# Kernel optimization log

Hardware: AMD Instinct MI355X
Metric: run time of the kernel (lower is better)

## Reference

```python
import jax, jax.numpy as jnp
import numpy as np

N = 4096
F_IN = 512
F_OUT = 64
H = 8
ALPHA = 0.2
NEG_BIG = -9e15


def setup_inputs() -> dict:
    key = jax.random.key(0)
    ks = jax.random.split(key, 7)
    h = jax.random.normal(ks[0], (N, F_IN), dtype=jnp.float32)
    mask = jax.random.randint(ks[1], (N, N), 0, 2, dtype=jnp.int32)
    # per-head linear W: weight [H, F_IN, F_OUT], bias [H, F_OUT] (xavier-ish scale)
    w_scale = 1.414 * np.sqrt(6.0 / (F_IN + F_OUT))
    W = jax.random.uniform(ks[2], (H, F_IN, F_OUT), dtype=jnp.float32, minval=-w_scale, maxval=w_scale)
    bW = jnp.zeros((H, F_OUT), dtype=jnp.float32)
    # attention linear A: [2*F_OUT, 1] split into a_l (acts on Wh_i) and a_r (acts on Wh_j)
    a_scale = 1.414 * np.sqrt(6.0 / (2 * F_OUT + 1))
    a_l = jax.random.uniform(ks[3], (H, F_OUT), dtype=jnp.float32, minval=-a_scale, maxval=a_scale)
    a_r = jax.random.uniform(ks[4], (H, F_OUT), dtype=jnp.float32, minval=-a_scale, maxval=a_scale)
    bA = jnp.zeros((H,), dtype=jnp.float32)
    return {"h": h, "mask": mask, "W": W, "bW": bW, "a_l": a_l, "a_r": a_r, "bA": bA}


def reference(h, mask, W, bW, a_l, a_r, bA):
    # Wh: [H, N, F_OUT]
    Wh = jnp.einsum('ni,hio->hno', h, W) + bW[:, None, :]
    # A([Wh_i ; Wh_j]) decomposed as outer sum: e[h,i,j] = a_l.Wh_i + a_r.Wh_j + bA
    el = jnp.einsum('hno,ho->hn', Wh, a_l)  # [H, N]
    er = jnp.einsum('hno,ho->hn', Wh, a_r)  # [H, N]
    e = el[:, :, None] + er[:, None, :] + bA[:, None, None]  # [H, N, N]
    e = jax.nn.leaky_relu(e, negative_slope=ALPHA)
    e = jnp.where(mask[None] > 0, e, NEG_BIG)
    a = jax.nn.softmax(e, axis=-1)  # softmax over neighbors j (dim=1 in torch)
    # dropout omitted (eval mode / deterministic reference)
    aWh = jnp.einsum('hij,hjo->hio', a, Wh)  # [H, N, F_OUT]
    out = jax.nn.elu(aWh)  # last=False
    # concat heads along feature dim -> [N, H*F_OUT]
    return jnp.transpose(out, (1, 0, 2)).reshape(N, H * F_OUT)
```

## Files before the change

kernel.cpp:

```cpp
#include <hip/hip_runtime.h>
#include <hip/hip_bf16.h>
#include <hip/hip_fp16.h>

#define NN 4096
#define FIN 512
#define FOUT 64
#define NH 8
#define ALPHA 0.2f
#define PSCALE 4096.0f

typedef unsigned int uint;
typedef unsigned short ushort;
typedef unsigned char uchar;
typedef unsigned long long ull;
typedef __attribute__((ext_vector_type(8))) short short8;
typedef __attribute__((ext_vector_type(8))) _Float16 half8;
typedef __attribute__((ext_vector_type(4))) float floatx4;
typedef __attribute__((ext_vector_type(4))) uint uintx4;
typedef __attribute__((ext_vector_type(2))) uint uintx2;

__device__ __forceinline__ float bf2f(ushort s) { return __uint_as_float(((uint)s) << 16); }
__device__ __forceinline__ ushort f2bf(float f) {
    uint u = __float_as_uint(f);
    u += 0x7fffu + ((u >> 16) & 1u);
    return (ushort)(u >> 16);
}
__device__ __forceinline__ ushort f2h(float f) {
    return __half_as_ushort(__float2half_rn(f));
}

__device__ __forceinline__ int detect_bf16(const ushort* __restrict__ hraw) {
    int lane = threadIdx.x & 63;
    float a = fabsf(bf2f(hraw[2 * lane]));
    ull bal = __ballot(a >= 1e-3f && a <= 100.0f);
    return __popcll(bal) >= 32;
}

#define PM_BLKS 8192
#define CV_BLKS 1024
#define TW_BLKS 32

__global__ __launch_bounds__(256) void prep_kernel(
    const int* __restrict__ mask, uchar* __restrict__ mb,
    const void* __restrict__ hraw, ushort* __restrict__ bh,
    const void* __restrict__ Wraw, ushort* __restrict__ WT)
{
    const int b = blockIdx.x, t = threadIdx.x;
    if (b < PM_BLKS) {
        size_t gid = (size_t)b * 256 + t;
        const int* p = mask + gid * 8;
        int4 aa = *(const int4*)p;
        int4 bb = *(const int4*)(p + 4);
        uint by = (uint)(aa.x > 0)        | ((uint)(aa.y > 0) << 1)
                | ((uint)(aa.z > 0) << 2) | ((uint)(aa.w > 0) << 3)
                | ((uint)(bb.x > 0) << 4) | ((uint)(bb.y > 0) << 5)
                | ((uint)(bb.z > 0) << 6) | ((uint)(bb.w > 0) << 7);
        mb[gid] = (uchar)by;
    } else if (b < PM_BLKS + CV_BLKS) {
        int isbf = detect_bf16((const ushort*)hraw);
        size_t e0 = ((size_t)(b - PM_BLKS) * 256 + t) * 8;
        if (isbf) {
            *(uint4*)(bh + e0) = *(const uint4*)((const ushort*)hraw + e0);
        } else {
            const float* s = (const float*)hraw + e0;
            float4 f0 = *(const float4*)s;
            float4 f1 = *(const float4*)(s + 4);
            uint4 o;
            o.x = (uint)f2bf(f0.x) | ((uint)f2bf(f0.y) << 16);
            o.y = (uint)f2bf(f0.z) | ((uint)f2bf(f0.w) << 16);
            o.z = (uint)f2bf(f1.x) | ((uint)f2bf(f1.y) << 16);
            o.w = (uint)f2bf(f1.z) | ((uint)f2bf(f1.w) << 16);
            *(uint4*)(bh + e0) = o;
        }
    } else {
        int isbf = detect_bf16((const ushort*)hraw);
        int b2 = b - PM_BLKS - CV_BLKS;
        int h = b2 >> 2, kq = b2 & 3;
        int o = t & 63, sub = t >> 6;
        int kbase = kq * 128 + sub * 32;
        uint pk[16];
#pragma unroll
        for (int kk = 0; kk < 32; kk += 2) {
            float v0, v1;
            size_t s0 = ((size_t)h * FIN + kbase + kk) * FOUT + o;
            size_t s1 = s0 + FOUT;
            if (isbf) { v0 = bf2f(((const ushort*)Wraw)[s0]); v1 = bf2f(((const ushort*)Wraw)[s1]); }
            else      { v0 = ((const float*)Wraw)[s0];        v1 = ((const float*)Wraw)[s1]; }
            pk[kk >> 1] = (uint)f2bf(v0) | ((uint)f2bf(v1) << 16);
        }
        ushort* dst = WT + ((size_t)h * FOUT + o) * FIN + kbase;
#pragma unroll
        for (int q = 0; q < 4; q++)
            *(uint4*)(dst + q * 8) = make_uint4(pk[q*4], pk[q*4+1], pk[q*4+2], pk[q*4+3]);
    }
}

__global__ __launch_bounds__(256) void khv_kernel(const float* __restrict__ er,
                                                  float* __restrict__ Kh,
                                                  ushort* __restrict__ vt,
                                                  ushort* __restrict__ zt) {
    __shared__ float red[256];
    int h = blockIdx.x >> 3, sl = blockIdx.x & 7, t = threadIdx.x;
    float m = -3.0e38f;
    for (int j = t; j < NN; j += 256) m = fmaxf(m, er[(size_t)h * NN + j]);
    red[t] = m;
    __syncthreads();
    for (int s = 128; s >= 1; s >>= 1) {
        if (t < s) red[t] = fmaxf(red[t], red[t + s]);
        __syncthreads();
    }
    float kh = red[0];
    if (t == 0 && sl == 0) Kh[h] = kh;
    int j = sl * 512 + t;
#pragma unroll
    for (int q = 0; q < 2; q++, j += 256) {
        float d = er[(size_t)h * NN + j] - kh;
        vt[(size_t)h * NN + j] = f2h(__expf(d));
        zt[(size_t)h * NN + j] = f2h(__expf(ALPHA * d));
    }
}

__global__ __launch_bounds__(256) void wh_kernel(
    const ushort* __restrict__ hmat, const ushort* __restrict__ WT,
    const void* __restrict__ bWr, const void* __restrict__ alr,
    const void* __restrict__ arr, const void* __restrict__ bAr,
    const ushort* __restrict__ hraw,
    ushort* __restrict__ WhT, float* __restrict__ el, float* __restrict__ er)
{
    __shared__ __align__(16) ushort sT[64][72];
    const int t = threadIdx.x, lane = t & 63, wid = t >> 6;
    const int head = blockIdx.y, rbase = blockIdx.x * 64;
    const int lm = lane & 15, lq = lane >> 4;

    floatx4 C[4];
#pragma unroll
    for (int cg = 0; cg < 4; cg++) C[cg] = (floatx4){0.f, 0.f, 0.f, 0.f};

    const ushort* Ap = hmat + (size_t)(rbase + wid * 16 + lm) * FIN + lq * 8;
    const ushort* Bp = WT + (size_t)head * FOUT * FIN + (size_t)lm * FIN + lq * 8;

#pragma unroll
    for (int kc = 0; kc < 16; kc++) {
        short8 a = *(const short8*)(Ap + kc * 32);
#pragma unroll
        for (int cg = 0; cg < 4; cg++) {
            short8 b = *(const short8*)(Bp + (size_t)cg * 16 * FIN + kc * 32);
            C[cg] = __builtin_amdgcn_mfma_f32_16x16x32_bf16(a, b, C[cg], 0, 0, 0);
        }
    }

    const int isbf = detect_bf16(hraw);
    float bA = isbf ? bf2f(((const ushort*)bAr)[head]) : ((const float*)bAr)[head];
    float pel[4] = {0.f, 0.f, 0.f, 0.f}, per[4] = {0.f, 0.f, 0.f, 0.f};
#pragma unroll
    for (int cg = 0; cg < 4; cg++) {
        int o = head * FOUT + cg * 16 + lm;
        float bw = isbf ? bf2f(((const ushort*)bWr)[o]) : ((const float*)bWr)[o];
        float av = isbf ? bf2f(((const ushort*)alr)[o]) : ((const float*)alr)[o];
        float rv = isbf ? bf2f(((const ushort*)arr)[o]) : ((const float*)arr)[o];
        ushort pk[4];
#pragma unroll
        for (int r = 0; r < 4; r++) {
            float v = C[cg][r] + bw;
            pel[r] += v * av;
            per[r] += v * rv;
            pk[r] = f2h(v);
        }
        ushort4 p4; p4.x = pk[0]; p4.y = pk[1]; p4.z = pk[2]; p4.w = pk[3];
        *(ushort4*)(&sT[cg * 16 + lm][wid * 16 + lq * 4]) = p4;
    }
#pragma unroll
    for (int off = 1; off < 16; off <<= 1) {
#pragma unroll
        for (int r = 0; r < 4; r++) {
            pel[r] += __shfl_xor(pel[r], off);
            per[r] += __shfl_xor(per[r], off);
        }
    }
    if (lm == 0) {
#pragma unroll
        for (int r = 0; r < 4; r++) {
            int row = rbase + wid * 16 + lq * 4 + r;
            el[(size_t)head * NN + row] = pel[r];
            er[(size_t)head * NN + row] = per[r] + bA;
        }
    }
    __syncthreads();
    {
        int o = t >> 2, ch = t & 3;
        uint4 v0 = *(const uint4*)(&sT[o][ch * 16]);
        uint4 v1 = *(const uint4*)(&sT[o][ch * 16 + 8]);
        ushort* d = WhT + ((size_t)head * FOUT + o) * NN + rbase + ch * 16;
        *(uint4*)d = v0;
        *(uint4*)(d + 8) = v1;
    }
}

__device__ __forceinline__ uint pkmul(uint a, uint b) {
    uint d; asm("v_pk_mul_f16 %0,%1,%2" : "=v"(d) : "v"(a), "v"(b)); return d;
}
__device__ __forceinline__ uint pkmax(uint a, uint b) {
    uint d; asm("v_pk_max_f16 %0,%1,%2" : "=v"(d) : "v"(a), "v"(b)); return d;
}
__device__ __forceinline__ uint pmask2(uint a) {
    uint b = a & 3u;
    return ((b | (b << 15)) & 0x10001u) * 0xFFFFu;
}
__device__ __forceinline__ half8 pgen8h(uintx4 vv, uintx4 zz, uint mby,
                                        uint uip, uint wip) {
    union { uintx4 u; half8 h; } c;
    c.u.x = pkmax(pkmul(uip, vv.x), pkmul(wip, zz.x)) & pmask2(mby);
    c.u.y = pkmax(pkmul(uip, vv.y), pkmul(wip, zz.y)) & pmask2(mby >> 2);
    c.u.z = pkmax(pkmul(uip, vv.z), pkmul(wip, zz.z)) & pmask2(mby >> 4);
    c.u.w = pkmax(pkmul(uip, vv.w), pkmul(wip, zz.w)) & pmask2(mby >> 6);
    return c.h;
}

#define KEEP(x) asm volatile("" : "+v"(x))
#define BARRIER() do { asm volatile("s_waitcnt lgkmcnt(0)" ::: "memory"); \
                       __builtin_amdgcn_s_barrier(); } while (0)

#define VZLOAD(S, j0) do {                                   \
    v##S##a = *(const uintx4*)(gvt + (j0) + sh8);            \
    v##S##b = *(const uintx4*)(gvt + (j0) + 32 + sh8);       \
    z##S##a = *(const uintx4*)(gzt + (j0) + sh8);            \
    z##S##b = *(const uintx4*)(gzt + (j0) + 32 + sh8);       \
} while (0)

__global__ __launch_bounds__(256, 2) void attn_kernel(
    const uchar* __restrict__ mb,
    const ushort* __restrict__ WhT,
    const float* __restrict__ el, const float* __restrict__ Kh,
    const ushort* __restrict__ vt, const ushort* __restrict__ zt,
    const ushort* __restrict__ hraw,
    void* __restrict__ outv)
{
    __shared__ __align__(16) ushort sB[2][2][64 * 72];

    const int t = threadIdx.x, lane = t & 63, wid = t >> 6;
    const int rg = wid >> 1;
    const int jh = wid & 1;
    const int b = blockIdx.x;
    const int head = b & 7;
    const int ibase = (b >> 3) * 64;
    const int lm = lane & 15, lq = lane >> 4;
    const int sh8 = lq * 8;

    const float kh = Kh[head];
    const int rowa = ibase + rg * 32 + lm;
    const float xa = el[(size_t)head * NN + rowa] + kh;
    const float xb = el[(size_t)head * NN + rowa + 16] + kh;
    const float Ma = fmaxf(xa, ALPHA * xa);
    const float Mb = fmaxf(xb, ALPHA * xb);
    const uint uipa = (uint)f2h(PSCALE * __expf(xa - Ma)) * 0x10001u;
    const uint wipa = (uint)f2h(PSCALE * __expf(ALPHA * xa - Ma)) * 0x10001u;
    const uint uipb = (uint)f2h(PSCALE * __expf(xb - Mb)) * 0x10001u;
    const uint wipb = (uint)f2h(PSCALE * __expf(ALPHA * xb - Mb)) * 0x10001u;

    const int jb = jh * 2048;
    const int st = rg * 64 + lane;
    const int so = st >> 1;
    const int sc = (st & 1) * 32;
    const ushort* gB = WhT + ((size_t)head * FOUT + so) * NN + jb + sc;
    const ushort* gvt = vt + (size_t)head * NN + jb;
    const ushort* gzt = zt + (size_t)head * NN + jb;
    const uchar* mra = mb + (size_t)rowa * 512 + (jb >> 3);
    const uchar* mrb = mra + 16 * 512;

    uintx4 rr0, rr1, rr2, rr3;
    uintx2 mka_s, mkb_s;

    auto gload = [&](int j0) {
        rr0 = *(const uintx4*)(gB + j0);
        rr1 = *(const uintx4*)(gB + j0 + 8);
        rr2 = *(const uintx4*)(gB + j0 + 16);
        rr3 = *(const uintx4*)(gB + j0 + 24);
        mka_s = *(const uintx2*)(mra + (j0 >> 3));
        mkb_s = *(const uintx2*)(mrb + (j0 >> 3));
    };
    auto lwrite = [&](int buf) {
        ushort* d = &sB[jh][buf][so * 72 + sc];
        *(uintx4*)(d)      = rr0;
        *(uintx4*)(d + 8)  = rr1;
        *(uintx4*)(d + 16) = rr2;
        *(uintx4*)(d + 24) = rr3;
    };

    uintx4 v0a, v0b, z0a, z0b;
    uintx4 v1a, v1b, z1a, z1b;

    const half8 onesh = {(_Float16)1.f, (_Float16)1.f, (_Float16)1.f, (_Float16)1.f,
                         (_Float16)1.f, (_Float16)1.f, (_Float16)1.f, (_Float16)1.f};
    floatx4 Z = {0.f, 0.f, 0.f, 0.f};
    floatx4 C0 = Z, C1 = Z, C2 = Z, C3 = Z, Cd0 = Z;
    floatx4 C4 = Z, C5 = Z, C6 = Z, C7 = Z, Cd1 = Z;

    auto compute = [&](int buf, uintx2 mka, uintx2 mkb,
                       uintx4 vA, uintx4 vB, uintx4 zA, uintx4 zB) {
        uint m0a = mka.x >> sh8;
        uint m1a = mka.y >> sh8;
        uint m0b = mkb.x >> sh8;
        uint m1b = mkb.y >> sh8;
        half8 a0 = pgen8h(vA, zA, m0a, uipa, wipa);
        half8 a1 = pgen8h(vB, zB, m1a, uipa, wipa);
        half8 a2 = pgen8h(vA, zA, m0b, uipb, wipb);
        half8 a3 = pgen8h(vB, zB, m1b, uipb, wipb);
        const ushort* base = &sB[jh][buf][0];
        half8 b00 = *(const half8*)(base + (0  + lm) * 72 + sh8);
        half8 b10 = *(const half8*)(base + (16 + lm) * 72 + sh8);
        half8 b20 = *(const half8*)(base + (32 + lm) * 72 + sh8);
        half8 b30 = *(const half8*)(base + (48 + lm) * 72 + sh8);
        Cd0 = __builtin_amdgcn_mfma_f32_16x16x32_f16(a0, onesh, Cd0, 0, 0, 0);
        Cd1 = __builtin_amdgcn_mfma_f32_16x16x32_f16(a2, onesh, Cd1, 0, 0, 0);
        C0 = __builtin_amdgcn_mfma_f32_16x16x32_f16(a0, b00, C0, 0, 0, 0);
        C4 = __builtin_amdgcn_mfma_f32_16x16x32_f16(a2, b00, C4, 0, 0, 0);
        C1 = __builtin_amdgcn_mfma_f32_16x16x32_f16(a0, b10, C1, 0, 0, 0);
        C5 = __builtin_amdgcn_mfma_f32_16x16x32_f16(a2, b10, C5, 0, 0, 0);
        C2 = __builtin_amdgcn_mfma_f32_16x16x32_f16(a0, b20, C2, 0, 0, 0);
        C6 = __builtin_amdgcn_mfma_f32_16x16x32_f16(a2, b20, C6, 0, 0, 0);
        C3 = __builtin_amdgcn_mfma_f32_16x16x32_f16(a0, b30, C3, 0, 0, 0);
        C7 = __builtin_amdgcn_mfma_f32_16x16x32_f16(a2, b30, C7, 0, 0, 0);
        half8 b01 = *(const half8*)(base + (0  + lm) * 72 + 32 + sh8);
        half8 b11 = *(const half8*)(base + (16 + lm) * 72 + 32 + sh8);
        half8 b21 = *(const half8*)(base + (32 + lm) * 72 + 32 + sh8);
        half8 b31 = *(const half8*)(base + (48 + lm) * 72 + 32 + sh8);
        Cd0 = __builtin_amdgcn_mfma_f32_16x16x32_f16(a1, onesh, Cd0, 0, 0, 0);
        Cd1 = __builtin_amdgcn_mfma_f32_16x16x32_f16(a3, onesh, Cd1, 0, 0, 0);
        C0 = __builtin_amdgcn_mfma_f32_16x16x32_f16(a1, b01, C0, 0, 0, 0);
        C4 = __builtin_amdgcn_mfma_f32_16x16x32_f16(a3, b01, C4, 0, 0, 0);
        C1 = __builtin_amdgcn_mfma_f32_16x16x32_f16(a1, b11, C1, 0, 0, 0);
        C5 = __builtin_amdgcn_mfma_f32_16x16x32_f16(a3, b11, C5, 0, 0, 0);
        C2 = __builtin_amdgcn_mfma_f32_16x16x32_f16(a1, b21, C2, 0, 0, 0);
        C6 = __builtin_amdgcn_mfma_f32_16x16x32_f16(a3, b21, C6, 0, 0, 0);
        C3 = __builtin_amdgcn_mfma_f32_16x16x32_f16(a1, b31, C3, 0, 0, 0);
        C7 = __builtin_amdgcn_mfma_f32_16x16x32_f16(a3, b31, C7, 0, 0, 0);
    };

    uintx2 mka0, mkb0, mka1, mkb1;
    gload(0);
    lwrite(0);
    mka0 = mka_s; mkb0 = mkb_s;
    gload(64);
    VZLOAD(0, 0);
    KEEP(rr0); KEEP(rr1); KEEP(rr2); KEEP(rr3);
    KEEP(v0a); KEEP(v0b); KEEP(z0a); KEEP(z0b);
    BARRIER();

    for (int it = 0; it < 32; it += 2) {
        lwrite(1);
        mka1 = mka_s; mkb1 = mkb_s;
        gload(((it + 2) & 31) * 64);
        VZLOAD(1, (it + 1) * 64);
        compute(0, mka0, mkb0, v0a, v0b, z0a, z0b);
        KEEP(v1a); KEEP(v1b); KEEP(z1a); KEEP(z1b);
        KEEP(rr0); KEEP(rr1); KEEP(rr2); KEEP(rr3);
        BARRIER();
        lwrite(0);
        mka0 = mka_s; mkb0 = mkb_s;
        gload(((it + 3) & 31) * 64);
        VZLOAD(0, ((it + 2) & 31) * 64);
        compute(1, mka1, mkb1, v1a, v1b, z1a, z1b);
        KEEP(v0a); KEEP(v0b); KEEP(z0a); KEEP(z0b);
        KEEP(rr0); KEEP(rr1); KEEP(rr2); KEEP(rr3);
        BARRIER();
    }

    float* mg = (float*)&sB[0][0][0];
    const int mi = (rg * 64 + lane) * 44;
    if (jh == 1) {
        float* p = &mg[mi];
        *(floatx4*)(p + 0)  = C0;  *(floatx4*)(p + 4)  = C1;
        *(floatx4*)(p + 8)  = C2;  *(floatx4*)(p + 12) = C3;
        *(floatx4*)(p + 16) = C4;  *(floatx4*)(p + 20) = C5;
        *(floatx4*)(p + 24) = C6;  *(floatx4*)(p + 28) = C7;
        *(floatx4*)(p + 32) = Cd0; *(floatx4*)(p + 36) = Cd1;
    }
    BARRIER();
    if (jh == 0) {
        const float* p = &mg[mi];
        C0 += *(const floatx4*)(p + 0);   C1 += *(const floatx4*)(p + 4);
        C2 += *(const floatx4*)(p + 8);   C3 += *(const floatx4*)(p + 12);
        C4 += *(const floatx4*)(p + 16);  C5 += *(const floatx4*)(p + 20);
        C6 += *(const floatx4*)(p + 24);  C7 += *(const floatx4*)(p + 28);
        Cd0 += *(const floatx4*)(p + 32); Cd1 += *(const floatx4*)(p + 36);

        const int isbf = detect_bf16(hraw);
#pragma unroll
        for (int r = 0; r < 4; r++) {
            int ra = ibase + rg * 32 + lq * 4 + r;
            int rb = ra + 16;
            float inva = 1.f / Cd0[r];
            float invb = 1.f / Cd1[r];
            float x0 = C0[r] * inva; x0 = (x0 > 0.f) ? x0 : __expf(x0) - 1.f;
            float x1 = C1[r] * inva; x1 = (x1 > 0.f) ? x1 : __expf(x1) - 1.f;
            float x2 = C2[r] * inva; x2 = (x2 > 0.f) ? x2 : __expf(x2) - 1.f;
            float x3 = C3[r] * inva; x3 = (x3 > 0.f) ? x3 : __expf(x3) - 1.f;
            float y0 = C4[r] * invb; y0 = (y0 > 0.f) ? y0 : __expf(y0) - 1.f;
            float y1 = C5[r] * invb; y1 = (y1 > 0.f) ? y1 : __expf(y1) - 1.f;
            float y2 = C6[r] * invb; y2 = (y2 > 0.f) ? y2 : __expf(y2) - 1.f;
            float y3 = C7[r] * invb; y3 = (y3 > 0.f) ? y3 : __expf(y3) - 1.f;
            size_t basea = (size_t)ra * (NH * FOUT) + head * FOUT + lm;
            size_t baseb = (size_t)rb * (NH * FOUT) + head * FOUT + lm;
            if (isbf) {
                ushort* o = (ushort*)outv;
                o[basea + 0]  = f2bf(x0);
                o[basea + 16] = f2bf(x1);
                o[basea + 32] = f2bf(x2);
                o[basea + 48] = f2bf(x3);
                o[baseb + 0]  = f2bf(y0);
                o[baseb + 16] = f2bf(y1);
                o[baseb + 32] = f2bf(y2);
                o[baseb + 48] = f2bf(y3);
            } else {
                float* o = (float*)outv;
                o[basea + 0]  = x0;
                o[basea + 16] = x1;
                o[basea + 32] = x2;
                o[basea + 48] = x3;
                o[baseb + 0]  = y0;
                o[baseb + 16] = y1;
                o[baseb + 32] = y2;
                o[baseb + 48] = y3;
            }
        }
    }
}

extern "C" void kernel_launch(void* const* d_in, const int* in_sizes, int n_in,
                              void* d_out, int out_size, void* d_ws, size_t ws_size,
                              hipStream_t stream)
{
    const void* hraw = d_in[0];
    const int*  mask = (const int*)d_in[1];
    const void* Wraw = d_in[2];
    const void* bWr  = d_in[3];
    const void* alr  = d_in[4];
    const void* arr  = d_in[5];
    const void* bAr  = d_in[6];

    char* w = (char*)d_ws;
    ushort* bh   = (ushort*)w;                  w += (size_t)NN * FIN * 2;
    ushort* WT   = (ushort*)w;                  w += (size_t)NH * FOUT * FIN * 2;
    ushort* WhT  = (ushort*)w;                  w += (size_t)NH * FOUT * NN * 2;
    float*  el   = (float*)w;                   w += (size_t)NH * NN * 4;
    float*  er   = (float*)w;                   w += (size_t)NH * NN * 4;
    float*  Kh   = (float*)w;                   w += 64;
    ushort* vt   = (ushort*)w;                  w += (size_t)NH * NN * 4;
    ushort* zt   = (ushort*)w;                  w += (size_t)NH * NN * 4;
    uchar*  mb   = (uchar*)w;                   w += (size_t)NN * 512;

    prep_kernel<<<PM_BLKS + CV_BLKS + TW_BLKS, 256, 0, stream>>>(
        mask, mb, hraw, bh, Wraw, WT);
    wh_kernel<<<dim3(NN / 64, NH), 256, 0, stream>>>(bh, WT, bWr, alr, arr, bAr,
                                                     (const ushort*)hraw, WhT, el, er);
    khv_kernel<<<64, 256, 0, stream>>>(er, Kh, vt, zt);
    attn_kernel<<<NN / 64 * NH, 256, 0, stream>>>(mb, WhT, el, Kh, vt, zt,
                                                  (const ushort*)hraw, d_out);
}
```

Measured before the change: 177.7 us.

## Split attention j-range across four waves per row group and switch Wh GEMM to fp16

```diff
diff --git a/kernel.cpp b/kernel.cpp
--- a/kernel.cpp
+++ b/kernel.cpp
@@ -86,7 +86,7 @@
             size_t s1 = s0 + FOUT;
             if (isbf) { v0 = bf2f(((const ushort*)Wraw)[s0]); v1 = bf2f(((const ushort*)Wraw)[s1]); }
             else      { v0 = ((const float*)Wraw)[s0];        v1 = ((const float*)Wraw)[s1]; }
-            pk[kk >> 1] = (uint)f2bf(v0) | ((uint)f2bf(v1) << 16);
+            pk[kk >> 1] = (uint)f2h(v0) | ((uint)f2h(v1) << 16);
         }
         ushort* dst = WT + ((size_t)h * FOUT + o) * FIN + kbase;
 #pragma unroll
@@ -141,11 +141,18 @@
 
 #pragma unroll
     for (int kc = 0; kc < 16; kc++) {
-        short8 a = *(const short8*)(Ap + kc * 32);
+        half8 a;
+        {
+            short8 ab = *(const short8*)(Ap + kc * 32);
+            union { ushort u[8]; half8 h; } cv;
+#pragma unroll
+            for (int e = 0; e < 8; e++) cv.u[e] = f2h(bf2f(((ushort*)&ab)[e]));
+            a = cv.h;
+        }
 #pragma unroll
         for (int cg = 0; cg < 4; cg++) {
-            short8 b = *(const short8*)(Bp + (size_t)cg * 16 * FIN + kc * 32);
-            C[cg] = __builtin_amdgcn_mfma_f32_16x16x32_bf16(a, b, C[cg], 0, 0, 0);
+            half8 bfr = *(const half8*)(Bp + (size_t)cg * 16 * FIN + kc * 32);
+            C[cg] = __builtin_amdgcn_mfma_f32_16x16x32_f16(a, bfr, C[cg], 0, 0, 0);
         }
     }
 
@@ -227,7 +234,7 @@
     z##S##b = *(const uintx4*)(gzt + (j0) + 32 + sh8);       \
 } while (0)
 
-__global__ __launch_bounds__(256, 2) void attn_kernel(
+__global__ __launch_bounds__(512, 4) void attn_kernel(
     const uchar* __restrict__ mb,
     const ushort* __restrict__ WhT,
     const float* __restrict__ el, const float* __restrict__ Kh,
@@ -235,11 +242,11 @@
     const ushort* __restrict__ hraw,
     void* __restrict__ outv)
 {
-    __shared__ __align__(16) ushort sB[2][2][64 * 72];
+    __shared__ __align__(16) ushort sB[4][2][64 * 72];
 
     const int t = threadIdx.x, lane = t & 63, wid = t >> 6;
-    const int rg = wid >> 1;
-    const int jh = wid & 1;
+    const int rg = wid >> 2;
+    const int jq = wid & 3;
     const int b = blockIdx.x;
     const int head = b & 7;
     const int ibase = (b >> 3) * 64;
@@ -257,7 +264,7 @@
     const uint uipb = (uint)f2h(PSCALE * __expf(xb - Mb)) * 0x10001u;
     const uint wipb = (uint)f2h(PSCALE * __expf(ALPHA * xb - Mb)) * 0x10001u;
 
-    const int jb = jh * 2048;
+    const int jb = jq * 1024;
     const int st = rg * 64 + lane;
     const int so = st >> 1;
     const int sc = (st & 1) * 32;
@@ -279,7 +286,7 @@
         mkb_s = *(const uintx2*)(mrb + (j0 >> 3));
     };
     auto lwrite = [&](int buf) {
-        ushort* d = &sB[jh][buf][so * 72 + sc];
+        ushort* d = &sB[jq][buf][so * 72 + sc];
         *(uintx4*)(d)      = rr0;
         *(uintx4*)(d + 8)  = rr1;
         *(uintx4*)(d + 16) = rr2;
@@ -305,7 +312,7 @@
         half8 a1 = pgen8h(vB, zB, m1a, uipa, wipa);
         half8 a2 = pgen8h(vA, zA, m0b, uipb, wipb);
         half8 a3 = pgen8h(vB, zB, m1b, uipb, wipb);
-        const ushort* base = &sB[jh][buf][0];
+        const ushort* base = &sB[jq][buf][0];
         half8 b00 = *(const half8*)(base + (0  + lm) * 72 + sh8);
         half8 b10 = *(const half8*)(base + (16 + lm) * 72 + sh8);
         half8 b20 = *(const half8*)(base + (32 + lm) * 72 + sh8);
@@ -346,10 +353,10 @@
     KEEP(v0a); KEEP(v0b); KEEP(z0a); KEEP(z0b);
     BARRIER();
 
-    for (int it = 0; it < 32; it += 2) {
+    for (int it = 0; it < 16; it += 2) {
         lwrite(1);
         mka1 = mka_s; mkb1 = mkb_s;
-        gload(((it + 2) & 31) * 64);
+        gload(((it + 2) & 15) * 64);
         VZLOAD(1, (it + 1) * 64);
         compute(0, mka0, mkb0, v0a, v0b, z0a, z0b);
         KEEP(v1a); KEEP(v1b); KEEP(z1a); KEEP(z1b);
@@ -357,8 +364,8 @@
         BARRIER();
         lwrite(0);
         mka0 = mka_s; mkb0 = mkb_s;
-        gload(((it + 3) & 31) * 64);
-        VZLOAD(0, ((it + 2) & 31) * 64);
+        gload(((it + 3) & 15) * 64);
+        VZLOAD(0, ((it + 2) & 15) * 64);
         compute(1, mka1, mkb1, v1a, v1b, z1a, z1b);
         KEEP(v0a); KEEP(v0b); KEEP(z0a); KEEP(z0b);
         KEEP(rr0); KEEP(rr1); KEEP(rr2); KEEP(rr3);
@@ -366,8 +373,8 @@
     }
 
     float* mg = (float*)&sB[0][0][0];
-    const int mi = (rg * 64 + lane) * 44;
-    if (jh == 1) {
+    const int mi = ((jq - 1) * 128 + rg * 64 + lane) * 44;
+    if (jq > 0) {
         float* p = &mg[mi];
         *(floatx4*)(p + 0)  = C0;  *(floatx4*)(p + 4)  = C1;
         *(floatx4*)(p + 8)  = C2;  *(floatx4*)(p + 12) = C3;
@@ -376,14 +383,16 @@
         *(floatx4*)(p + 32) = Cd0; *(floatx4*)(p + 36) = Cd1;
     }
     BARRIER();
-    if (jh == 0) {
-        const float* p = &mg[mi];
-        C0 += *(const floatx4*)(p + 0);   C1 += *(const floatx4*)(p + 4);
-        C2 += *(const floatx4*)(p + 8);   C3 += *(const floatx4*)(p + 12);
-        C4 += *(const floatx4*)(p + 16);  C5 += *(const floatx4*)(p + 20);
-        C6 += *(const floatx4*)(p + 24);  C7 += *(const floatx4*)(p + 28);
-        Cd0 += *(const floatx4*)(p + 32); Cd1 += *(const floatx4*)(p + 36);
-
+    if (jq == 0) {
+#pragma unroll
+        for (int s = 0; s < 3; s++) {
+            const float* p = &mg[(s * 128 + rg * 64 + lane) * 44];
+            C0 += *(const floatx4*)(p + 0);   C1 += *(const floatx4*)(p + 4);
+            C2 += *(const floatx4*)(p + 8);   C3 += *(const floatx4*)(p + 12);
+            C4 += *(const floatx4*)(p + 16);  C5 += *(const floatx4*)(p + 20);
+            C6 += *(const floatx4*)(p + 24);  C7 += *(const floatx4*)(p + 28);
+            Cd0 += *(const floatx4*)(p + 32); Cd1 += *(const floatx4*)(p + 36);
+        }
         const int isbf = detect_bf16(hraw);
 #pragma unroll
         for (int r = 0; r < 4; r++) {
@@ -454,6 +463,6 @@
     wh_kernel<<<dim3(NN / 64, NH), 256, 0, stream>>>(bh, WT, bWr, alr, arr, bAr,
                                                      (const ushort*)hraw, WhT, el, er);
     khv_kernel<<<64, 256, 0, stream>>>(er, Kh, vt, zt);
-    attn_kernel<<<NN / 64 * NH, 256, 0, stream>>>(mb, WhT, el, Kh, vt, zt,
+    attn_kernel<<<NN / 64 * NH, 512, 0, stream>>>(mb, WhT, el, Kh, vt, zt,
                                                   (const ushort*)hraw, d_out);
 }
```

Measured after the change: 194.0 us. 1.09x slower.
